# Kernel optimization log

Measured on AMD Instinct MI355X. Metric: run time of the kernel, lower is better.

The kernel has to match this reference:

```python
import jax, jax.numpy as jnp
import numpy as np

THRESHOLD = 1.0
BETA_INIT = 0.9

def setup_inputs() -> dict:
    key = jax.random.key(0)
    k1, k2 = jax.random.split(key)
    B, T, D, E = 16, 4096, 1024, 64
    seq = jax.random.normal(k1, (B, T, D), dtype=jnp.float32)
    W = jax.random.normal(k2, (E, D), dtype=jnp.float32) * (1.0 / np.sqrt(D))
    b = jnp.zeros((E,), dtype=jnp.float32)
    logit = float(np.log(BETA_INIT / (1.0 - BETA_INIT)))
    beta_raw = jnp.full((E,), logit, dtype=jnp.float32)
    return {"seq": seq, "W": W, "b": b, "beta_raw": beta_raw}

def reference(seq, W, b, beta_raw):
    # seq: [B,T,D], W: [E,D], b: [E], beta_raw: [E]
    B, T, D = seq.shape
    E = W.shape[0]
    beta = jax.nn.sigmoid(beta_raw)                       # [E]
    # batch the per-timestep Linear into one GEMM: [B,T,E]
    I = jnp.einsum('btd,ed->bte', seq, W) + b
    def step(U, I_t):
        U = beta * U + I_t                                # leaky integrate
        U = U - jax.nn.relu(U - THRESHOLD)                # soft reset (clip at threshold)
        return U, None
    U0 = jnp.zeros((B, E), dtype=seq.dtype)
    # scan over time: I transposed to [T,B,E]
    U_final, _ = jax.lax.scan(step, U0, jnp.swapaxes(I, 0, 1))
    return jax.nn.softmax(U_final, axis=-1)
```

## Files before the change

kernel.cpp:

```cpp
#include <hip/hip_runtime.h>
#include <hip/hip_bf16.h>
#include <cstdint>

#define B_ 16
#define T_ 4096
#define D_ 1024
#define E_ 64
#define THRESH 1.0f
#define MBLK 128
#define BK 32
#define NCH 32

typedef float f32x4 __attribute__((ext_vector_type(4)));
typedef short s16x8 __attribute__((ext_vector_type(8)));

typedef __attribute__((address_space(3))) void lds_void_t;
typedef const __attribute__((address_space(1))) void gbl_void_t;

__device__ __forceinline__ void split1(float v, unsigned short& h, unsigned short& l) {
    unsigned u = __float_as_uint(v);
    float hf = __uint_as_float(u & 0xFFFF0000u);
    float r = v - hf;
    h = (unsigned short)(u >> 16);
    l = (unsigned short)(__float_as_uint(r) >> 16);
}

__device__ __forceinline__ void split8(float4 v0, float4 v1, s16x8& h8, s16x8& l8) {
    unsigned short h0,h1,h2,h3,h4,h5,h6,h7, l0,l1,l2,l3,l4,l5,l6,l7;
    split1(v0.x,h0,l0); split1(v0.y,h1,l1); split1(v0.z,h2,l2); split1(v0.w,h3,l3);
    split1(v1.x,h4,l4); split1(v1.y,h5,l5); split1(v1.z,h6,l6); split1(v1.w,h7,l7);
    h8 = (s16x8){(short)h0,(short)h1,(short)h2,(short)h3,(short)h4,(short)h5,(short)h6,(short)h7};
    l8 = (s16x8){(short)l0,(short)l1,(short)l2,(short)l3,(short)l4,(short)l5,(short)l6,(short)l7};
}

__global__ void wconv_kernel(const float* __restrict__ W,
                             unsigned short* __restrict__ Whi,
                             unsigned short* __restrict__ Wlo) {
    int i = (blockIdx.x * 256 + threadIdx.x) * 4;
    if (i >= E_ * D_) return;
    float4 v = *reinterpret_cast<const float4*>(W + i);
    ushort4 h, l;
    split1(v.x, h.x, l.x); split1(v.y, h.y, l.y);
    split1(v.z, h.z, l.z); split1(v.w, h.w, l.w);
    *reinterpret_cast<ushort4*>(Whi + i) = h;
    *reinterpret_cast<ushort4*>(Wlo + i) = l;
}

__device__ __forceinline__ int swz128(int row, int cb) {
    return cb ^ ((row & 3) << 5) ^ (((row >> 2) & 1) << 4);
}

__global__ __launch_bounds__(256, 2) void lif_gemm_kernel(
    const float* __restrict__ seq,
    const unsigned short* __restrict__ Whi, const unsigned short* __restrict__ Wlo,
    const float* __restrict__ bias, const float* __restrict__ beta_raw,
    float* __restrict__ Cw, float* __restrict__ Mw)
{
    __shared__ __align__(16) unsigned char lds[49152];
    unsigned char* const A0 = lds;
    unsigned char* const A1 = lds + 16384;
    unsigned char* const W0 = lds + 32768;
    unsigned char* const W1 = lds + 40960;

    const int tid  = threadIdx.x;
    const int wave = tid >> 6;
    const int lane = tid & 63;
    const int c = lane & 15;
    const int q = lane >> 4;
    const long row0 = (long)blockIdx.x * MBLK;

    auto stage = [&](unsigned char* Ab, unsigned char* Wb, int k0) {
        #pragma unroll
        for (int i = 0; i < 4; ++i) {
            int o16 = i * 256 + wave * 64 + lane;
            int row = o16 >> 3;
            int cb  = (o16 & 7) << 4;
            int cbs = swz128(row, cb);
            gbl_void_t* src = (gbl_void_t*)(seq + (row0 + row) * D_ + k0 + (cbs >> 2));
            lds_void_t* dst = (lds_void_t*)(Ab + (i * 256 + wave * 64) * 16);
            __builtin_amdgcn_global_load_lds(src, dst, 16, 0, 0);
        }
        #pragma unroll
        for (int i = 0; i < 2; ++i) {
            int o16 = i * 256 + wave * 64 + lane;
            int row = o16 >> 3;
            int cb  = (o16 & 7) << 4;
            int cbs = swz128(row, cb);
            const unsigned short* wsrc = (cbs < 64) ? Whi : Wlo;
            gbl_void_t* src = (gbl_void_t*)(wsrc + row * D_ + k0 + ((cbs & 63) >> 1));
            lds_void_t* dst = (lds_void_t*)(Wb + (i * 256 + wave * 64) * 16);
            __builtin_amdgcn_global_load_lds(src, dst, 16, 0, 0);
        }
    };

    f32x4 acc[2][4] = {};

    auto compute = [&](const unsigned char* Ab, const unsigned char* Wb) {
        s16x8 ah[2], al[2], bh[4], bl[4];
        #pragma unroll
        for (int m = 0; m < 2; ++m) {
            int r = wave * 32 + m * 16 + c;
            float4 v0 = *(const float4*)(Ab + r * 128 + swz128(r, q * 32));
            float4 v1 = *(const float4*)(Ab + r * 128 + swz128(r, q * 32 + 16));
            split8(v0, v1, ah[m], al[m]);
        }
        #pragma unroll
        for (int n = 0; n < 4; ++n) {
            int r = n * 16 + c;
            bh[n] = *(const s16x8*)(Wb + r * 128 + swz128(r, q * 16));
            bl[n] = *(const s16x8*)(Wb + r * 128 + swz128(r, 64 + q * 16));
        }
        #pragma unroll
        for (int m = 0; m < 2; ++m)
            #pragma unroll
            for (int n = 0; n < 4; ++n)
                acc[m][n] = __builtin_amdgcn_mfma_f32_16x16x32_bf16(ah[m], bh[n], acc[m][n], 0, 0, 0);
        #pragma unroll
        for (int m = 0; m < 2; ++m)
            #pragma unroll
            for (int n = 0; n < 4; ++n)
                acc[m][n] = __builtin_amdgcn_mfma_f32_16x16x32_bf16(al[m], bh[n], acc[m][n], 0, 0, 0);
        #pragma unroll
        for (int m = 0; m < 2; ++m)
            #pragma unroll
            for (int n = 0; n < 4; ++n)
                acc[m][n] = __builtin_amdgcn_mfma_f32_16x16x32_bf16(ah[m], bl[n], acc[m][n], 0, 0, 0);
    };

    stage(A0, W0, 0);
    stage(A1, W1, BK);

    for (int t = 0; t < NCH - 2; t += 2) {
        asm volatile("s_waitcnt vmcnt(6)" ::: "memory");
        __builtin_amdgcn_s_barrier();
        compute(A0, W0);
        asm volatile("s_waitcnt lgkmcnt(0)" ::: "memory");
        __builtin_amdgcn_s_barrier();
        stage(A0, W0, (t + 2) * BK);

        asm volatile("s_waitcnt vmcnt(6)" ::: "memory");
        __builtin_amdgcn_s_barrier();
        compute(A1, W1);
        asm volatile("s_waitcnt lgkmcnt(0)" ::: "memory");
        __builtin_amdgcn_s_barrier();
        stage(A1, W1, (t + 3) * BK);
    }
    asm volatile("s_waitcnt vmcnt(6)" ::: "memory");
    __builtin_amdgcn_s_barrier();
    compute(A0, W0);
    asm volatile("s_waitcnt lgkmcnt(0)" ::: "memory");
    __builtin_amdgcn_s_barrier();
    asm volatile("s_waitcnt vmcnt(0)" ::: "memory");
    __builtin_amdgcn_s_barrier();
    compute(A1, W1);

    float beta[4], A4[4], A8[4], bi[4];
    #pragma unroll
    for (int n = 0; n < 4; ++n) {
        beta[n] = 1.0f / (1.0f + __expf(-beta_raw[n * 16 + c]));
        float b2 = beta[n] * beta[n];
        A4[n] = b2 * b2;
        A8[n] = A4[n] * A4[n];
        bi[n] = bias[n * 16 + c];
    }

    float C[2][4], M[2][4];
    #pragma unroll
    for (int m = 0; m < 2; ++m)
        #pragma unroll
        for (int n = 0; n < 4; ++n) {
            float Cc = 0.0f, Mm = 3.0e38f;
            #pragma unroll
            for (int r = 0; r < 4; ++r) {
                float v = acc[m][n][r] + bi[n];
                Cc = fmaf(beta[n], Cc, v);
                Mm = fminf(fmaf(beta[n], Mm, v), THRESH);
            }
            C[m][n] = Cc; M[m][n] = Mm;
        }

    #pragma unroll
    for (int m = 0; m < 2; ++m)
        #pragma unroll
        for (int n = 0; n < 4; ++n) {
            {
                float Cp = __shfl_xor(C[m][n], 16, 64);
                float Mp = __shfl_xor(M[m][n], 16, 64);
                bool sf = (lane & 16) == 0;
                float Cf = sf ? C[m][n] : Cp, Cs = sf ? Cp : C[m][n];
                float Mf = sf ? M[m][n] : Mp, Ms = sf ? Mp : M[m][n];
                C[m][n] = fmaf(A4[n], Cf, Cs);
                M[m][n] = fminf(fmaf(A4[n], Mf, Cs), Ms);
            }
            {
                float Cp = __shfl_xor(C[m][n], 32, 64);
                float Mp = __shfl_xor(M[m][n], 32, 64);
                bool sf = (lane & 32) == 0;
                float Cf = sf ? C[m][n] : Cp, Cs = sf ? Cp : C[m][n];
                float Mf = sf ? M[m][n] : Mp, Ms = sf ? Mp : M[m][n];
                C[m][n] = fmaf(A8[n], Cf, Cs);
                M[m][n] = fminf(fmaf(A8[n], Mf, Cs), Ms);
            }
        }

    float Cm[4], Mm4[4];
    #pragma unroll
    for (int n = 0; n < 4; ++n) {
        float A16 = A8[n] * A8[n];
        Cm[n]  = fmaf(A16, C[0][n], C[1][n]);
        Mm4[n] = fminf(fmaf(A16, M[0][n], C[1][n]), M[1][n]);
    }

    float Co = (q == 0) ? Cm[0] : (q == 1) ? Cm[1] : (q == 2) ? Cm[2] : Cm[3];
    float Mo = (q == 0) ? Mm4[0] : (q == 1) ? Mm4[1] : (q == 2) ? Mm4[2] : Mm4[3];
    int sub = blockIdx.x * 4 + wave;
    Cw[sub * 64 + q * 16 + c] = Co;
    Mw[sub * 64 + q * 16 + c] = Mo;
}

__global__ void lif_combine_kernel(const float* __restrict__ Cw, const float* __restrict__ Mw,
                                   const float* __restrict__ beta_raw, float* __restrict__ out)
{
    __shared__ float Cs[4][64], Ms[4][64];
    const int b = blockIdx.x;
    const int wv = threadIdx.x >> 6;
    const int e  = threadIdx.x & 63;

    float beta = 1.0f / (1.0f + __expf(-beta_raw[e]));
    float A32 = beta * beta;
    A32 = A32 * A32;
    A32 = A32 * A32;
    A32 = A32 * A32;
    A32 = A32 * A32;

    const float* Cp = Cw + ((size_t)b * 128 + wv * 32) * 64 + e;
    const float* Mp = Mw + ((size_t)b * 128 + wv * 32) * 64 + e;
    float Cc = Cp[0], Mm = Mp[0];
    #pragma unroll 8
    for (int i = 1; i < 32; ++i) {
        float ci = Cp[i * 64], mi = Mp[i * 64];
        Mm = fminf(fmaf(A32, Mm, ci), mi);
        Cc = fmaf(A32, Cc, ci);
    }
    Cs[wv][e] = Cc; Ms[wv][e] = Mm;
    __syncthreads();

    if (threadIdx.x < 64) {
        float Ag = A32;
        Ag = Ag * Ag; Ag = Ag * Ag; Ag = Ag * Ag; Ag = Ag * Ag; Ag = Ag * Ag;
        float C0 = Cs[0][e], M0 = Ms[0][e];
        #pragma unroll
        for (int g = 1; g < 4; ++g) {
            float ci = Cs[g][e], mi = Ms[g][e];
            M0 = fminf(fmaf(Ag, M0, ci), mi);
            C0 = fmaf(Ag, C0, ci);
        }
        float U = fminf(C0, M0);
        float m = U;
        #pragma unroll
        for (int off = 32; off; off >>= 1) m = fmaxf(m, __shfl_xor(m, off, 64));
        float ex = __expf(U - m);
        float s = ex;
        #pragma unroll
        for (int off = 32; off; off >>= 1) s += __shfl_xor(s, off, 64);
        out[b * 64 + e] = ex / s;
    }
}

extern "C" void kernel_launch(void* const* d_in, const int* in_sizes, int n_in,
                              void* d_out, int out_size, void* d_ws, size_t ws_size,
                              hipStream_t stream)
{
    const float* seq  = (const float*)d_in[0];
    const float* W    = (const float*)d_in[1];
    const float* bias = (const float*)d_in[2];
    const float* braw = (const float*)d_in[3];
    float* out = (float*)d_out;

    char* ws = (char*)d_ws;
    unsigned short* Whi = (unsigned short*)ws;
    unsigned short* Wlo = (unsigned short*)(ws + 131072);
    float* Cw = (float*)(ws + 262144);
    float* Mw = (float*)(ws + 786432);

    wconv_kernel<<<64, 256, 0, stream>>>(W, Whi, Wlo);
    lif_gemm_kernel<<<(B_ * T_) / MBLK, 256, 0, stream>>>(seq, Whi, Wlo, bias, braw, Cw, Mw);
    lif_combine_kernel<<<B_, 256, 0, stream>>>(Cw, Mw, braw, out);
}
```

Baseline: 55.91 us.

## Fuse weight split and combine stage into single GEMM kernel via last-block reduction

Removes the separate weight-conversion kernel: W is now staged in fp32 and split into bf16 hi/lo in registers inside the GEMM loop. Removes the separate combine kernel: each block bumps an atomic counter, and the last block scans all per-chunk partial states and computes the softmax. This saves two kernel launches and the Whi/Wlo round trip through memory. In exchange it adds a memset launch, per-iteration VALU work to split W, and a serial combine tail that runs in only one block.

```diff
diff --git a/kernel.cpp b/kernel.cpp
--- a/kernel.cpp
+++ b/kernel.cpp
@@ -10,6 +10,7 @@
 #define MBLK 128
 #define BK 32
 #define NCH 32
+#define GRID 512
 
 typedef float f32x4 __attribute__((ext_vector_type(4)));
 typedef short s16x8 __attribute__((ext_vector_type(8)));
@@ -33,28 +34,15 @@
     l8 = (s16x8){(short)l0,(short)l1,(short)l2,(short)l3,(short)l4,(short)l5,(short)l6,(short)l7};
 }
 
-__global__ void wconv_kernel(const float* __restrict__ W,
-                             unsigned short* __restrict__ Whi,
-                             unsigned short* __restrict__ Wlo) {
-    int i = (blockIdx.x * 256 + threadIdx.x) * 4;
-    if (i >= E_ * D_) return;
-    float4 v = *reinterpret_cast<const float4*>(W + i);
-    ushort4 h, l;
-    split1(v.x, h.x, l.x); split1(v.y, h.y, l.y);
-    split1(v.z, h.z, l.z); split1(v.w, h.w, l.w);
-    *reinterpret_cast<ushort4*>(Whi + i) = h;
-    *reinterpret_cast<ushort4*>(Wlo + i) = l;
-}
-
 __device__ __forceinline__ int swz128(int row, int cb) {
     return cb ^ ((row & 3) << 5) ^ (((row >> 2) & 1) << 4);
 }
 
-__global__ __launch_bounds__(256, 2) void lif_gemm_kernel(
-    const float* __restrict__ seq,
-    const unsigned short* __restrict__ Whi, const unsigned short* __restrict__ Wlo,
+__global__ __launch_bounds__(256, 2) void lif_fused_kernel(
+    const float* __restrict__ seq, const float* __restrict__ Wg,
     const float* __restrict__ bias, const float* __restrict__ beta_raw,
-    float* __restrict__ Cw, float* __restrict__ Mw)
+    float* __restrict__ Cw, float* __restrict__ Mw,
+    int* __restrict__ cnt, float* __restrict__ out)
 {
     __shared__ __align__(16) unsigned char lds[49152];
     unsigned char* const A0 = lds;
@@ -86,8 +74,7 @@
             int row = o16 >> 3;
             int cb  = (o16 & 7) << 4;
             int cbs = swz128(row, cb);
-            const unsigned short* wsrc = (cbs < 64) ? Whi : Wlo;
-            gbl_void_t* src = (gbl_void_t*)(wsrc + row * D_ + k0 + ((cbs & 63) >> 1));
+            gbl_void_t* src = (gbl_void_t*)(Wg + row * D_ + k0 + (cbs >> 2));
             lds_void_t* dst = (lds_void_t*)(Wb + (i * 256 + wave * 64) * 16);
             __builtin_amdgcn_global_load_lds(src, dst, 16, 0, 0);
         }
@@ -107,8 +94,9 @@
         #pragma unroll
         for (int n = 0; n < 4; ++n) {
             int r = n * 16 + c;
-            bh[n] = *(const s16x8*)(Wb + r * 128 + swz128(r, q * 16));
-            bl[n] = *(const s16x8*)(Wb + r * 128 + swz128(r, 64 + q * 16));
+            float4 w0 = *(const float4*)(Wb + r * 128 + swz128(r, q * 32));
+            float4 w1 = *(const float4*)(Wb + r * 128 + swz128(r, q * 32 + 16));
+            split8(w0, w1, bh[n], bl[n]);
         }
         #pragma unroll
         for (int m = 0; m < 2; ++m)
@@ -216,54 +204,49 @@
     int sub = blockIdx.x * 4 + wave;
     Cw[sub * 64 + q * 16 + c] = Co;
     Mw[sub * 64 + q * 16 + c] = Mo;
-}
-
-__global__ void lif_combine_kernel(const float* __restrict__ Cw, const float* __restrict__ Mw,
-                                   const float* __restrict__ beta_raw, float* __restrict__ out)
-{
-    __shared__ float Cs[4][64], Ms[4][64];
-    const int b = blockIdx.x;
-    const int wv = threadIdx.x >> 6;
-    const int e  = threadIdx.x & 63;
-
-    float beta = 1.0f / (1.0f + __expf(-beta_raw[e]));
-    float A32 = beta * beta;
-    A32 = A32 * A32;
-    A32 = A32 * A32;
-    A32 = A32 * A32;
-    A32 = A32 * A32;
-
-    const float* Cp = Cw + ((size_t)b * 128 + wv * 32) * 64 + e;
-    const float* Mp = Mw + ((size_t)b * 128 + wv * 32) * 64 + e;
-    float Cc = Cp[0], Mm = Mp[0];
-    #pragma unroll 8
-    for (int i = 1; i < 32; ++i) {
-        float ci = Cp[i * 64], mi = Mp[i * 64];
-        Mm = fminf(fmaf(A32, Mm, ci), mi);
-        Cc = fmaf(A32, Cc, ci);
-    }
-    Cs[wv][e] = Cc; Ms[wv][e] = Mm;
+
+    __threadfence();
     __syncthreads();
-
-    if (threadIdx.x < 64) {
-        float Ag = A32;
-        Ag = Ag * Ag; Ag = Ag * Ag; Ag = Ag * Ag; Ag = Ag * Ag; Ag = Ag * Ag;
-        float C0 = Cs[0][e], M0 = Ms[0][e];
-        #pragma unroll
-        for (int g = 1; g < 4; ++g) {
-            float ci = Cs[g][e], mi = Ms[g][e];
-            M0 = fminf(fmaf(Ag, M0, ci), mi);
-            C0 = fmaf(Ag, C0, ci);
-        }
-        float U = fminf(C0, M0);
-        float m = U;
-        #pragma unroll
-        for (int off = 32; off; off >>= 1) m = fmaxf(m, __shfl_xor(m, off, 64));
-        float ex = __expf(U - m);
-        float s = ex;
-        #pragma unroll
-        for (int off = 32; off; off >>= 1) s += __shfl_xor(s, off, 64);
-        out[b * 64 + e] = ex / s;
+    __shared__ int is_last;
+    if (tid == 0) {
+        int prev = atomicAdd(cnt, 1);
+        is_last = (prev == GRID - 1);
+    }
+    __syncthreads();
+    if (!is_last) return;
+    __threadfence();
+
+    {
+        float betaE = 1.0f / (1.0f + __expf(-beta_raw[lane]));
+        float A32 = betaE * betaE;
+        A32 = A32 * A32;
+        A32 = A32 * A32;
+        A32 = A32 * A32;
+        A32 = A32 * A32;
+        #pragma unroll
+        for (int i = 0; i < 4; ++i) {
+            int b = wave * 4 + i;
+            const float* Cp = Cw + ((size_t)b * 128) * 64 + lane;
+            const float* Mp = Mw + ((size_t)b * 128) * 64 + lane;
+            float Cc = __hip_atomic_load(&Cp[0], __ATOMIC_RELAXED, __HIP_MEMORY_SCOPE_AGENT);
+            float Mm = __hip_atomic_load(&Mp[0], __ATOMIC_RELAXED, __HIP_MEMORY_SCOPE_AGENT);
+            #pragma unroll 8
+            for (int ch = 1; ch < 128; ++ch) {
+                float ci = __hip_atomic_load(&Cp[ch * 64], __ATOMIC_RELAXED, __HIP_MEMORY_SCOPE_AGENT);
+                float mi = __hip_atomic_load(&Mp[ch * 64], __ATOMIC_RELAXED, __HIP_MEMORY_SCOPE_AGENT);
+                Mm = fminf(fmaf(A32, Mm, ci), mi);
+                Cc = fmaf(A32, Cc, ci);
+            }
+            float U = fminf(Cc, Mm);
+            float mx = U;
+            #pragma unroll
+            for (int off = 32; off; off >>= 1) mx = fmaxf(mx, __shfl_xor(mx, off, 64));
+            float ex = __expf(U - mx);
+            float s = ex;
+            #pragma unroll
+            for (int off = 32; off; off >>= 1) s += __shfl_xor(s, off, 64);
+            out[b * 64 + lane] = ex / s;
+        }
     }
 }
 
@@ -278,12 +261,10 @@
     float* out = (float*)d_out;
 
     char* ws = (char*)d_ws;
-    unsigned short* Whi = (unsigned short*)ws;
-    unsigned short* Wlo = (unsigned short*)(ws + 131072);
-    float* Cw = (float*)(ws + 262144);
-    float* Mw = (float*)(ws + 786432);
-
-    wconv_kernel<<<64, 256, 0, stream>>>(W, Whi, Wlo);
-    lif_gemm_kernel<<<(B_ * T_) / MBLK, 256, 0, stream>>>(seq, Whi, Wlo, bias, braw, Cw, Mw);
-    lif_combine_kernel<<<B_, 256, 0, stream>>>(Cw, Mw, braw, out);
-}
+    float* Cw = (float*)ws;
+    float* Mw = (float*)(ws + 524288);
+    int*   cnt = (int*)(ws + 1048576);
+
+    hipMemsetAsync(cnt, 0, 4, stream);
+    lif_fused_kernel<<<GRID, 256, 0, stream>>>(seq, W, bias, braw, Cw, Mw, cnt, out);
+}
```

After: 134.2 us. 2.4x slower.
